# Kernel tuning notes

Hardware: AMD Instinct MI355X
Metric: run time of the kernel (lower is better)

The kernel has to match this reference:

```python
import jax, jax.numpy as jnp
import numpy as np

C = 32            # multiplicity per irrep (node irreps = 32x0e + 32x1o)
N_NODES = 50000
N_EDGES = 800000
R_DIM = 8         # radial embedding dim
R_HID = 8         # radial MLP hidden width
N_SPECIES = 5
AVG_NEIGH = 16.0
N_PATHS = 4       # 0ex0e->0e, 0ex1o->1o, 1ox0e->1o, 1ox1o->0e


def setup_inputs() -> dict:
    key = jax.random.key(0)
    ks = jax.random.split(key, 16)
    inp = {
        'node_features': jax.random.normal(ks[0], (N_NODES, 4 * C), jnp.float32),
        'edge_features': jax.random.normal(ks[1], (N_EDGES, 4), jnp.float32),
        'radial_embedding': jax.random.normal(ks[2], (N_EDGES, R_DIM), jnp.float32),
        'senders': jax.random.randint(ks[3], (N_EDGES,), 0, N_NODES),
        'receivers': jax.random.randint(ks[4], (N_EDGES,), 0, N_NODES),
        'node_species': jax.random.randint(ks[5], (N_NODES,), 0, N_SPECIES),
        # linear_up: per-irrep (block-diagonal) mixing
        'W_up_s': jax.random.normal(ks[6], (C, C), jnp.float32),
        'W_up_v': jax.random.normal(ks[7], (C, C), jnp.float32),
        # radial MLP (no biases, e3nn-style): R_DIM -> R_HID -> N_PATHS*C
        'W_r1': jax.random.normal(ks[8], (R_DIM, R_HID), jnp.float32),
        'W_r2': jax.random.normal(ks[9], (R_HID, N_PATHS * C), jnp.float32),
        # linear_down: 2C x 0e -> 2C (C feats + C gates); 2C x 1o -> C x 1o
        'W_down_s': jax.random.normal(ks[10], (2 * C, 2 * C), jnp.float32),
        'W_down_v': jax.random.normal(ks[11], (2 * C, C), jnp.float32),
        # species-indexed skip connection to gate irreps
        'W_skip_s': jax.random.normal(ks[12], (N_SPECIES, C, 2 * C), jnp.float32),
        'W_skip_v': jax.random.normal(ks[13], (N_SPECIES, C, C), jnp.float32),
    }
    return inp


def reference(node_features, edge_features, radial_embedding, senders, receivers,
              node_species, W_up_s, W_up_v, W_r1, W_r2, W_down_s, W_down_v,
              W_skip_s, W_skip_v):
    N = node_features.shape[0]
    inv_sqrt_C = 1.0 / np.sqrt(C)
    # split irreps: scalars [N,C] and vectors [N,C,3]
    s = node_features[:, :C]
    v = node_features[:, C:].reshape(N, C, 3)
    # ---- linear_up (block-diagonal irreps Linear, fan-in normalized) ----
    s_up = (s @ W_up_s) * inv_sqrt_C
    v_up = jnp.einsum('ncx,cd->ndx', v, W_up_v) * inv_sqrt_C
    # ---- radial MLP -> per-edge tensor-product path weights ----
    h = jax.nn.silu((radial_embedding @ W_r1) * (1.0 / np.sqrt(R_DIM)))
    w = ((h @ W_r2) * (1.0 / np.sqrt(R_HID))).reshape(-1, N_PATHS, C)  # [E,4,C]
    # ---- tensor product messages over edges ----
    sh0 = edge_features[:, 0]      # [E]  l=0
    sh1 = edge_features[:, 1:4]    # [E,3] l=1
    se = s_up[senders]             # [E,C]
    ve = v_up[senders]             # [E,C,3]
    m0 = jnp.concatenate([
        w[:, 0] * se * sh0[:, None],                                      # 0e x 0e -> 0e
        w[:, 3] * jnp.einsum('ecx,ex->ec', ve, sh1) * (1.0 / np.sqrt(3.0))  # 1o x 1o -> 0e
    ], axis=1)                                                            # [E,2C]
    m1 = jnp.concatenate([
        w[:, 1, :, None] * se[:, :, None] * sh1[:, None, :],              # 0e x 1o -> 1o
        w[:, 2, :, None] * ve * sh0[:, None, None],                       # 1o x 0e -> 1o
    ], axis=1)                                                            # [E,2C,3]
    # ---- scatter aggregate to receivers, normalize by sqrt(avg neigh) ----
    inv_sqrt_deg = 1.0 / np.sqrt(AVG_NEIGH)
    agg0 = jax.ops.segment_sum(m0, receivers, num_segments=N) * inv_sqrt_deg
    agg1 = jax.ops.segment_sum(m1, receivers, num_segments=N) * inv_sqrt_deg
    # ---- linear_down to gate irreps (2C x 0e: C feats + C gates; C x 1o) ----
    inv_sqrt_2C = 1.0 / np.sqrt(2 * C)
    sc = (agg0 @ W_down_s) * inv_sqrt_2C                     # [N,2C]
    vc = jnp.einsum('ncx,cd->ndx', agg1, W_down_v) * inv_sqrt_2C  # [N,C,3]
    # ---- species-indexed skip connection ----
    skip_s = jnp.einsum('nc,ncd->nd', s, W_skip_s[node_species]) * inv_sqrt_C
    skip_v = jnp.einsum('ncx,ncd->ndx', v, W_skip_v[node_species]) * inv_sqrt_C
    sc = 0.5 * (sc + skip_s)
    vc = 0.5 * (vc + skip_v)
    # ---- gated nonlinearity: silu on scalars, silu(gates) * vectors ----
    feats = jax.nn.silu(sc[:, :C])
    gates = jax.nn.silu(sc[:, C:])
    vg = vc * gates[:, :, None]
    return jnp.concatenate([feats, vg.reshape(N, 3 * C)], axis=1)  # [N,4C]
```

## Files before the change

kernel.cpp:

```cpp
#include <hip/hip_runtime.h>
#include <stdint.h>

__device__ __forceinline__ float b2f(unsigned short u) {
    union { uint32_t i; float f; } v; v.i = ((uint32_t)u) << 16; return v.f;
}
__device__ __forceinline__ unsigned short f2b(float f) {
    union { float f; uint32_t i; } v; v.f = f;
    uint32_t i = v.i;
    uint32_t r = (i + 0x7fffu + ((i >> 16) & 1u)) >> 16;
    return (unsigned short)r;
}
__device__ __forceinline__ float silu_f(float x) { return x / (1.f + __expf(-x)); }

template<bool BF>
__device__ __forceinline__ float ldin(const void* p, size_t i) {
    if (BF) return b2f(((const unsigned short*)p)[i]);
    return ((const float*)p)[i];
}
template<bool BF>
__device__ __forceinline__ void ld4(const void* p, size_t i, float o[4]) {
    if (BF) {
        const ushort4 u = *(const ushort4*)((const unsigned short*)p + i);
        o[0] = b2f(u.x); o[1] = b2f(u.y); o[2] = b2f(u.z); o[3] = b2f(u.w);
    } else {
        const float4 f = *(const float4*)((const float*)p + i);
        o[0] = f.x; o[1] = f.y; o[2] = f.z; o[3] = f.w;
    }
}
template<bool BF>
__device__ __forceinline__ void stout(void* p, size_t i, float v) {
    if (BF) ((unsigned short*)p)[i] = f2b(v);
    else    ((float*)p)[i] = v;
}

#define INV_SQRT_C   0.17677669529663687f
#define INV_SQRT_8   0.3535533905932738f
#define INV_SQRT_3   0.5773502691896258f
#define INV_SQRT_DEG 0.25f
#define INV_SQRT_2C  0.125f

__device__ __forceinline__ bool detect_bf(const void* nf) {
    const int lane = threadIdx.x & 63;
    const uint32_t w = ((const uint32_t*)nf)[lane];
    const uint32_t ex = (w >> 7) & 0xFFu;
    const unsigned long long m = __ballot(ex >= 96u && ex <= 130u);
    return __popcll(m) > 32;
}

template<bool BF>
__device__ __forceinline__ void prep_body(
    const void* __restrict__ nf, const void* __restrict__ Wus,
    const void* __restrict__ Wuv, const void* __restrict__ radial,
    const int* __restrict__ recv, const void* __restrict__ Wr1,
    unsigned short* __restrict__ stage, unsigned short* __restrict__ hbuf,
    int* __restrict__ counts, int* __restrict__ table,
    int* __restrict__ ovcnt, int* __restrict__ ovlist, int N, int E)
{
    __shared__ float wsm[4][128];
    const int wave = threadIdx.x >> 6;
    const int lane = threadIdx.x & 63;
    const int nwaves = gridDim.x * 4;
    for (int n = blockIdx.x * 4 + wave; n < N; n += nwaves) {
        wsm[wave][lane]      = ldin<BF>(nf, (size_t)n * 128 + lane);
        wsm[wave][64 + lane] = ldin<BF>(nf, (size_t)n * 128 + 64 + lane);
        if (lane < 32) {
            float acc = 0.f;
            #pragma unroll 8
            for (int c = 0; c < 32; ++c) acc += wsm[wave][c] * ldin<BF>(Wus, c * 32 + lane);
            stage[(size_t)n * 160 + lane] = f2b(acc * INV_SQRT_C);
        } else {
            const int dd = lane - 32;
            float ax = 0.f, ay = 0.f, az = 0.f;
            #pragma unroll 8
            for (int c = 0; c < 32; ++c) {
                const float wv = ldin<BF>(Wuv, c * 32 + dd);
                ax += wsm[wave][32 + 3 * c    ] * wv;
                ay += wsm[wave][32 + 3 * c + 1] * wv;
                az += wsm[wave][32 + 3 * c + 2] * wv;
            }
            *(ushort4*)(stage + (size_t)n * 160 + 32 + 4 * dd) =
                make_ushort4(f2b(ax * INV_SQRT_C), f2b(ay * INV_SQRT_C),
                             f2b(az * INV_SQRT_C), (unsigned short)0);
        }
    }
    for (int e = blockIdx.x * 256 + threadIdx.x; e < E; e += gridDim.x * 256) {
        const int rr = recv[e];
        const int pos = atomicAdd(&counts[rr], 1);
        float r[8];
        ld4<BF>(radial, (size_t)e * 8, r);
        ld4<BF>(radial, (size_t)e * 8 + 4, r + 4);
        unsigned short h[8];
        #pragma unroll
        for (int j = 0; j < 8; ++j) {
            float pre = 0.f;
            #pragma unroll
            for (int k = 0; k < 8; ++k) pre += r[k] * ldin<BF>(Wr1, k * 8 + j);
            h[j] = f2b(silu_f(pre * INV_SQRT_8) * INV_SQRT_8);
        }
        ushort4* hp = (ushort4*)(hbuf + (size_t)e * 8);
        hp[0] = make_ushort4(h[0], h[1], h[2], h[3]);
        hp[1] = make_ushort4(h[4], h[5], h[6], h[7]);
        if (pos < 64) table[(size_t)rr * 64 + pos] = e;
        else          ovlist[atomicAdd(ovcnt, 1)] = e;
    }
}
__global__ __launch_bounds__(256) void k_prep(
    const void* nf, const void* Wus, const void* Wuv, const void* radial,
    const int* recv, const void* Wr1,
    unsigned short* stage, unsigned short* hbuf,
    int* counts, int* table, int* ovcnt, int* ovlist, int N, int E)
{
    if (detect_bf(nf)) prep_body<true >(nf, Wus, Wuv, radial, recv, Wr1, stage, hbuf,
                                        counts, table, ovcnt, ovlist, N, E);
    else               prep_body<false>(nf, Wus, Wuv, radial, recv, Wr1, stage, hbuf,
                                        counts, table, ovcnt, ovlist, N, E);
}

template<bool BF>
__device__ __forceinline__ void aggregate_body(
    const void* __restrict__ nf, const void* __restrict__ ef,
    const int* __restrict__ senders, const int* __restrict__ recv,
    const int* __restrict__ species,
    const void* __restrict__ Wr2, const void* __restrict__ Wds,
    const void* __restrict__ Wdv, const void* __restrict__ Wss,
    const void* __restrict__ Wsv,
    const unsigned short* __restrict__ stage,
    const unsigned short* __restrict__ hbuf,
    const int* __restrict__ counts, const int* __restrict__ table,
    const int* __restrict__ ovcnt, const int* __restrict__ ovlist,
    void* __restrict__ out, int N)
{
    __shared__ float ldsM[4][64][16];
    __shared__ float ldsNF[4][128];
    const int wave = threadIdx.x >> 6;
    const int lane = threadIdx.x & 63;
    const int n = blockIdx.x * 4 + wave;
    const bool valid = (n < N);
    const int d = lane - 32;
    int sp = 0, cnt = 0, mc = 0;
    float wA[8], wB[8];
    float acc0 = 0.f, a1x = 0.f, a1y = 0.f, a1z = 0.f;

    if (valid) {
        sp  = species[n];
        cnt = counts[n];
        mc  = (cnt < 64) ? cnt : 64;
        const int colA = (lane < 32) ? lane : lane + 32;
        #pragma unroll
        for (int j = 0; j < 8; ++j) {
            wA[j] = ldin<BF>(Wr2, j * 128 + colA);
            wB[j] = ldin<BF>(Wr2, j * 128 + colA + 32);
        }
        ldsNF[wave][lane]      = ldin<BF>(nf, (size_t)n * 128 + lane);
        ldsNF[wave][64 + lane] = ldin<BF>(nf, (size_t)n * 128 + 64 + lane);
        if (lane < mc) {
            const int eid = table[(size_t)n * 64 + lane];
            const int snd = senders[eid];
            float e4[4];
            if (BF) {
                const ushort4 u = *(const ushort4*)((const unsigned short*)ef + (size_t)eid * 4);
                e4[0] = b2f(u.x); e4[1] = b2f(u.y); e4[2] = b2f(u.z); e4[3] = b2f(u.w);
            } else {
                ld4<false>(ef, (size_t)eid * 4, e4);
            }
            const uint4 th = *(const uint4*)(hbuf + (size_t)eid * 8);
            float* M = ldsM[wave][lane];
            ((float4*)M)[0] = make_float4(e4[0], e4[1], e4[2], e4[3]);
            ((float4*)M)[1] = make_float4(b2f((unsigned short)(th.x & 0xFFFFu)),
                                          b2f((unsigned short)(th.x >> 16)),
                                          b2f((unsigned short)(th.y & 0xFFFFu)),
                                          b2f((unsigned short)(th.y >> 16)));
            ((float4*)M)[2] = make_float4(b2f((unsigned short)(th.z & 0xFFFFu)),
                                          b2f((unsigned short)(th.z >> 16)),
                                          b2f((unsigned short)(th.w & 0xFFFFu)),
                                          b2f((unsigned short)(th.w >> 16)));
            M[12] = __int_as_float(snd);
        }
    }

    if (valid && mc > 0) {
        auto gather = [&](int idx) -> ushort4 {
            const int snd = __float_as_int(ldsM[wave][idx][12]);
            const unsigned short* rec = stage + (size_t)snd * 160;
            if (lane < 32) return make_ushort4(rec[lane], (unsigned short)0,
                                               (unsigned short)0, (unsigned short)0);
            return *(const ushort4*)(rec + 32 + 4 * d);
        };
        ushort4 c0 = make_ushort4(0, 0, 0, 0), c1 = c0, c2 = c0;
        c0 = gather(0);
        if (mc > 1) c1 = gather(1);
        for (int i = 0; i < mc; ++i) {
            if (i + 2 < mc) c2 = gather(i + 2);
            const float4 e4 = ((const float4*)ldsM[wave][i])[0];
            const float4 ha = ((const float4*)ldsM[wave][i])[1];
            const float4 hb = ((const float4*)ldsM[wave][i])[2];
            const float vA = ha.x * wA[0] + ha.y * wA[1] + ha.z * wA[2] + ha.w * wA[3]
                           + hb.x * wA[4] + hb.y * wA[5] + hb.z * wA[6] + hb.w * wA[7];
            const float vB = ha.x * wB[0] + ha.y * wB[1] + ha.z * wB[2] + ha.w * wB[3]
                           + hb.x * wB[4] + hb.y * wB[5] + hb.z * wB[6] + hb.w * wB[7];
            const float sh0 = e4.x, s1x = e4.y, s1y = e4.z, s1z = e4.w;
            if (lane < 32) {
                const float se = b2f(c0.x);
                acc0 += vA * se * sh0;
                const float tt = vB * se;
                a1x += tt * s1x; a1y += tt * s1y; a1z += tt * s1z;
            } else {
                const float vx = b2f(c0.x), vy = b2f(c0.y), vz = b2f(c0.z);
                acc0 += vB * (vx * s1x + vy * s1y + vz * s1z) * INV_SQRT_3;
                const float tt = vA * sh0;
                a1x += tt * vx; a1y += tt * vy; a1z += tt * vz;
            }
            c0 = c1; c1 = c2;
        }
    }
    if (valid && cnt > 64) {
        const int oc = *ovcnt;
        for (int i2 = 0; i2 < oc; ++i2) {
            const int e = ovlist[i2];
            if (recv[e] != n) continue;
            const int s = senders[e];
            float efv[4];
            ld4<BF>(ef, (size_t)e * 4, efv);
            const float sh0 = efv[0], s1x = efv[1], s1y = efv[2], s1z = efv[3];
            float h[8];
            #pragma unroll
            for (int j = 0; j < 8; ++j) h[j] = b2f(hbuf[(size_t)e * 8 + j]);
            const float vA = h[0] * wA[0] + h[1] * wA[1] + h[2] * wA[2] + h[3] * wA[3]
                           + h[4] * wA[4] + h[5] * wA[5] + h[6] * wA[6] + h[7] * wA[7];
            const float vB = h[0] * wB[0] + h[1] * wB[1] + h[2] * wB[2] + h[3] * wB[3]
                           + h[4] * wB[4] + h[5] * wB[5] + h[6] * wB[6] + h[7] * wB[7];
            const unsigned short* rec = stage + (size_t)s * 160;
            if (lane < 32) {
                const float se = b2f(rec[lane]);
                acc0 += vA * se * sh0;
                const float tt = vB * se;
                a1x += tt * s1x; a1y += tt * s1y; a1z += tt * s1z;
            } else {
                const ushort4 u = *(const ushort4*)(rec + 32 + 4 * d);
                const float vx = b2f(u.x), vy = b2f(u.y), vz = b2f(u.z);
                acc0 += vB * (vx * s1x + vy * s1y + vz * s1z) * INV_SQRT_3;
                const float tt = vA * sh0;
                a1x += tt * vx; a1y += tt * vy; a1z += tt * vz;
            }
        }
    }

    __syncthreads();

    float* base = &ldsM[0][0][0];
    float (*lds_agg0)[64]    = (float(*)[64])   base;
    float (*lds_agg1)[3][65] = (float(*)[3][65])(base + 256);
    float (*lds_scf)[64]     = (float(*)[64])  (base + 1036);

    if (valid) {
        lds_agg0[wave][lane]    = acc0 * INV_SQRT_DEG;
        lds_agg1[wave][0][lane] = a1x * INV_SQRT_DEG;
        lds_agg1[wave][1][lane] = a1y * INV_SQRT_DEG;
        lds_agg1[wave][2][lane] = a1z * INV_SQRT_DEG;

        float sc = 0.f;
        #pragma unroll 8
        for (int c = 0; c < 64; ++c) sc += lds_agg0[wave][c] * ldin<BF>(Wds, c * 64 + lane);
        sc *= INV_SQRT_2C;
        float ss = 0.f;
        #pragma unroll 8
        for (int c = 0; c < 32; ++c)
            ss += ldsNF[wave][c] * ldin<BF>(Wss, (size_t)sp * 2048 + c * 64 + lane);
        ss *= INV_SQRT_C;
        lds_scf[wave][lane] = 0.5f * (sc + ss);

        #pragma unroll
        for (int rr = 0; rr < 2; ++rr) {
            const int p = lane + rr * 64;
            float outv;
            if (p < 32) {
                outv = silu_f(lds_scf[wave][p]);
            } else {
                const int o = p - 32;
                const int c = o / 3;
                const int x = o - 3 * c;
                float vc = 0.f;
                #pragma unroll 8
                for (int c2 = 0; c2 < 64; ++c2)
                    vc += lds_agg1[wave][x][c2] * ldin<BF>(Wdv, c2 * 32 + c);
                vc *= INV_SQRT_2C;
                float sv = 0.f;
                #pragma unroll 8
                for (int c2 = 0; c2 < 32; ++c2)
                    sv += ldsNF[wave][32 + c2 * 3 + x] * ldin<BF>(Wsv, (size_t)sp * 1024 + c2 * 32 + c);
                sv *= INV_SQRT_C;
                const float g = silu_f(lds_scf[wave][32 + c]);
                outv = 0.5f * (vc + sv) * g;
            }
            stout<BF>(out, (size_t)n * 128 + p, outv);
        }
    }
}
__global__ __launch_bounds__(256) void k_aggregate(
    const void* nf, const void* ef, const int* senders, const int* recv,
    const int* species,
    const void* Wr2, const void* Wds, const void* Wdv, const void* Wss, const void* Wsv,
    const unsigned short* stage, const unsigned short* hbuf,
    const int* counts, const int* table, const int* ovcnt, const int* ovlist,
    void* out, int N)
{
    if (detect_bf(nf)) aggregate_body<true >(nf, ef, senders, recv, species,
                                             Wr2, Wds, Wdv, Wss, Wsv,
                                             stage, hbuf, counts, table, ovcnt, ovlist, out, N);
    else               aggregate_body<false>(nf, ef, senders, recv, species,
                                             Wr2, Wds, Wdv, Wss, Wsv,
                                             stage, hbuf, counts, table, ovcnt, ovlist, out, N);
}

extern "C" void kernel_launch(void* const* d_in, const int* in_sizes, int n_in,
                              void* d_out, int out_size, void* d_ws, size_t ws_size,
                              hipStream_t stream) {
    const void* nf      = d_in[0];
    const void* ef      = d_in[1];
    const void* radial  = d_in[2];
    const int*  senders = (const int*)d_in[3];
    const int*  recv    = (const int*)d_in[4];
    const int*  specie  = (const int*)d_in[5];
    const void* Wus = d_in[6];
    const void* Wuv = d_in[7];
    const void* Wr1 = d_in[8];
    const void* Wr2 = d_in[9];
    const void* Wds = d_in[10];
    const void* Wdv = d_in[11];
    const void* Wss = d_in[12];
    const void* Wsv = d_in[13];

    const int N = in_sizes[5];
    const int E = in_sizes[3];

    const size_t stageB = (size_t)N * 160 * 2;
    const size_t hbufB  = (size_t)E * 8 * 2;
    const size_t tableB = (size_t)N * 64 * 4;
    const size_t need   = stageB + hbufB + tableB + (size_t)(N + 1 + E) * 4;
    if (ws_size < need) return;

    char* ws = (char*)d_ws;
    unsigned short* stage = (unsigned short*)ws;
    unsigned short* hbuf  = (unsigned short*)(ws + stageB);
    int* table   = (int*)(ws + stageB + hbufB);
    int* counts  = (int*)(ws + stageB + hbufB + tableB);
    int* ovcnt   = counts + N;
    int* ovlist  = ovcnt + 1;

    hipMemsetAsync(counts, 0, (size_t)(N + 1) * sizeof(int), stream);

    k_prep<<<2048, 256, 0, stream>>>(nf, Wus, Wuv, radial, recv, Wr1,
                                     stage, hbuf, counts, table, ovcnt, ovlist, N, E);
    k_aggregate<<<(N + 3) / 4, 256, 0, stream>>>(nf, ef, senders, recv, specie,
                                                 Wr2, Wds, Wdv, Wss, Wsv,
                                                 stage, hbuf, counts, table, ovcnt, ovlist,
                                                 d_out, N);
}
```

Before: 479.9 us.

## Split prep into node/edge kernels, shrink staging layout, batch sender gathers

```diff
diff --git a/kernel.cpp b/kernel.cpp
--- a/kernel.cpp
+++ b/kernel.cpp
@@ -39,81 +39,99 @@
 #define INV_SQRT_DEG 0.25f
 #define INV_SQRT_2C  0.125f
 
-__device__ __forceinline__ bool detect_bf(const void* nf) {
+__device__ __forceinline__ bool detect_bf(const void* buf) {
     const int lane = threadIdx.x & 63;
-    const uint32_t w = ((const uint32_t*)nf)[lane];
+    const uint32_t w = ((const uint32_t*)buf)[lane];
     const uint32_t ex = (w >> 7) & 0xFFu;
     const unsigned long long m = __ballot(ex >= 96u && ex <= 130u);
     return __popcll(m) > 32;
 }
 
 template<bool BF>
-__device__ __forceinline__ void prep_body(
+__device__ __forceinline__ void prep_nodes_body(
     const void* __restrict__ nf, const void* __restrict__ Wus,
-    const void* __restrict__ Wuv, const void* __restrict__ radial,
-    const int* __restrict__ recv, const void* __restrict__ Wr1,
-    unsigned short* __restrict__ stage, unsigned short* __restrict__ hbuf,
-    int* __restrict__ counts, int* __restrict__ table,
-    int* __restrict__ ovcnt, int* __restrict__ ovlist, int N, int E)
-{
-    __shared__ float wsm[4][128];
+    const void* __restrict__ Wuv, unsigned short* __restrict__ stage,
+    int N, float* smem)
+{
+    float (*wsm)[128] = (float(*)[128])smem;
     const int wave = threadIdx.x >> 6;
     const int lane = threadIdx.x & 63;
-    const int nwaves = gridDim.x * 4;
-    for (int n = blockIdx.x * 4 + wave; n < N; n += nwaves) {
-        wsm[wave][lane]      = ldin<BF>(nf, (size_t)n * 128 + lane);
-        wsm[wave][64 + lane] = ldin<BF>(nf, (size_t)n * 128 + 64 + lane);
-        if (lane < 32) {
-            float acc = 0.f;
-            #pragma unroll 8
-            for (int c = 0; c < 32; ++c) acc += wsm[wave][c] * ldin<BF>(Wus, c * 32 + lane);
-            stage[(size_t)n * 160 + lane] = f2b(acc * INV_SQRT_C);
-        } else {
-            const int dd = lane - 32;
-            float ax = 0.f, ay = 0.f, az = 0.f;
-            #pragma unroll 8
-            for (int c = 0; c < 32; ++c) {
-                const float wv = ldin<BF>(Wuv, c * 32 + dd);
-                ax += wsm[wave][32 + 3 * c    ] * wv;
-                ay += wsm[wave][32 + 3 * c + 1] * wv;
-                az += wsm[wave][32 + 3 * c + 2] * wv;
-            }
-            *(ushort4*)(stage + (size_t)n * 160 + 32 + 4 * dd) =
-                make_ushort4(f2b(ax * INV_SQRT_C), f2b(ay * INV_SQRT_C),
-                             f2b(az * INV_SQRT_C), (unsigned short)0);
-        }
-    }
-    for (int e = blockIdx.x * 256 + threadIdx.x; e < E; e += gridDim.x * 256) {
-        const int rr = recv[e];
-        const int pos = atomicAdd(&counts[rr], 1);
-        float r[8];
-        ld4<BF>(radial, (size_t)e * 8, r);
-        ld4<BF>(radial, (size_t)e * 8 + 4, r + 4);
-        unsigned short h[8];
+    const int n = blockIdx.x * 4 + wave;
+    if (n >= N) return;
+    wsm[wave][lane]      = ldin<BF>(nf, (size_t)n * 128 + lane);
+    wsm[wave][64 + lane] = ldin<BF>(nf, (size_t)n * 128 + 64 + lane);
+    if (lane < 32) {
+        float acc = 0.f;
+        #pragma unroll 8
+        for (int c = 0; c < 32; ++c) acc += wsm[wave][c] * ldin<BF>(Wus, c * 32 + lane);
+        stage[(size_t)n * 128 + lane] = f2b(acc * INV_SQRT_C);
+    } else {
+        const int dd = lane - 32;
+        float ax = 0.f, ay = 0.f, az = 0.f;
+        #pragma unroll 8
+        for (int c = 0; c < 32; ++c) {
+            const float wv = ldin<BF>(Wuv, c * 32 + dd);
+            ax += wsm[wave][32 + 3 * c    ] * wv;
+            ay += wsm[wave][32 + 3 * c + 1] * wv;
+            az += wsm[wave][32 + 3 * c + 2] * wv;
+        }
+        stage[(size_t)n * 128 + 32 + dd] = f2b(ax * INV_SQRT_C);
+        stage[(size_t)n * 128 + 64 + dd] = f2b(ay * INV_SQRT_C);
+        stage[(size_t)n * 128 + 96 + dd] = f2b(az * INV_SQRT_C);
+    }
+}
+__global__ __launch_bounds__(256) void k_prep_nodes(
+    const void* nf, const void* Wus, const void* Wuv,
+    unsigned short* stage, int N)
+{
+    __shared__ float smem[4 * 128];
+    if (detect_bf(nf)) prep_nodes_body<true >(nf, Wus, Wuv, stage, N, smem);
+    else               prep_nodes_body<false>(nf, Wus, Wuv, stage, N, smem);
+}
+
+template<bool BF>
+__device__ __forceinline__ void prep_edges_body(
+    const void* __restrict__ radial, const int* __restrict__ senders,
+    const int* __restrict__ recv, const void* __restrict__ Wr1,
+    unsigned short* __restrict__ hbuf, int* __restrict__ counts,
+    int* __restrict__ table, int* __restrict__ tableS,
+    int* __restrict__ ovcnt, int* __restrict__ ovlist, int E)
+{
+    const int e = blockIdx.x * 256 + threadIdx.x;
+    if (e >= E) return;
+    const int rr  = recv[e];
+    const int snd = senders[e];
+    const int pos = atomicAdd(&counts[rr], 1);
+    float r[8];
+    ld4<BF>(radial, (size_t)e * 8, r);
+    ld4<BF>(radial, (size_t)e * 8 + 4, r + 4);
+    unsigned short h[8];
+    #pragma unroll
+    for (int j = 0; j < 8; ++j) {
+        float pre = 0.f;
         #pragma unroll
-        for (int j = 0; j < 8; ++j) {
-            float pre = 0.f;
-            #pragma unroll
-            for (int k = 0; k < 8; ++k) pre += r[k] * ldin<BF>(Wr1, k * 8 + j);
-            h[j] = f2b(silu_f(pre * INV_SQRT_8) * INV_SQRT_8);
-        }
-        ushort4* hp = (ushort4*)(hbuf + (size_t)e * 8);
-        hp[0] = make_ushort4(h[0], h[1], h[2], h[3]);
-        hp[1] = make_ushort4(h[4], h[5], h[6], h[7]);
-        if (pos < 64) table[(size_t)rr * 64 + pos] = e;
-        else          ovlist[atomicAdd(ovcnt, 1)] = e;
-    }
-}
-__global__ __launch_bounds__(256) void k_prep(
-    const void* nf, const void* Wus, const void* Wuv, const void* radial,
-    const int* recv, const void* Wr1,
-    unsigned short* stage, unsigned short* hbuf,
-    int* counts, int* table, int* ovcnt, int* ovlist, int N, int E)
-{
-    if (detect_bf(nf)) prep_body<true >(nf, Wus, Wuv, radial, recv, Wr1, stage, hbuf,
-                                        counts, table, ovcnt, ovlist, N, E);
-    else               prep_body<false>(nf, Wus, Wuv, radial, recv, Wr1, stage, hbuf,
-                                        counts, table, ovcnt, ovlist, N, E);
+        for (int k = 0; k < 8; ++k) pre += r[k] * ldin<BF>(Wr1, k * 8 + j);
+        h[j] = f2b(silu_f(pre * INV_SQRT_8) * INV_SQRT_8);
+    }
+    ushort4* hp = (ushort4*)(hbuf + (size_t)e * 8);
+    hp[0] = make_ushort4(h[0], h[1], h[2], h[3]);
+    hp[1] = make_ushort4(h[4], h[5], h[6], h[7]);
+    if (pos < 64) {
+        table[(size_t)rr * 64 + pos] = e;
+        if (tableS) tableS[(size_t)rr * 64 + pos] = snd;
+    } else {
+        ovlist[atomicAdd(ovcnt, 1)] = e;
+    }
+}
+__global__ __launch_bounds__(256) void k_prep_edges(
+    const void* radial, const int* senders, const int* recv, const void* Wr1,
+    unsigned short* hbuf, int* counts, int* table, int* tableS,
+    int* ovcnt, int* ovlist, int E)
+{
+    if (detect_bf(radial)) prep_edges_body<true >(radial, senders, recv, Wr1, hbuf,
+                                                  counts, table, tableS, ovcnt, ovlist, E);
+    else                   prep_edges_body<false>(radial, senders, recv, Wr1, hbuf,
+                                                  counts, table, tableS, ovcnt, ovlist, E);
 }
 
 template<bool BF>
@@ -127,11 +145,12 @@
     const unsigned short* __restrict__ stage,
     const unsigned short* __restrict__ hbuf,
     const int* __restrict__ counts, const int* __restrict__ table,
+    const int* __restrict__ tableS,
     const int* __restrict__ ovcnt, const int* __restrict__ ovlist,
-    void* __restrict__ out, int N)
-{
-    __shared__ float ldsM[4][64][16];
-    __shared__ float ldsNF[4][128];
+    void* __restrict__ out, int N, float* smem)
+{
+    float (*ldsM)[64][16] = (float(*)[64][16])smem;
+    float (*ldsNF)[128]   = (float(*)[128])(smem + 4096);
     const int wave = threadIdx.x >> 6;
     const int lane = threadIdx.x & 63;
     const int n = blockIdx.x * 4 + wave;
@@ -155,7 +174,8 @@
         ldsNF[wave][64 + lane] = ldin<BF>(nf, (size_t)n * 128 + 64 + lane);
         if (lane < mc) {
             const int eid = table[(size_t)n * 64 + lane];
-            const int snd = senders[eid];
+            const int snd = tableS ? tableS[(size_t)n * 64 + lane]
+                                   : senders[eid];
             float e4[4];
             if (BF) {
                 const ushort4 u = *(const ushort4*)((const unsigned short*)ef + (size_t)eid * 4);
@@ -179,38 +199,48 @@
     }
 
     if (valid && mc > 0) {
-        auto gather = [&](int idx) -> ushort4 {
+        auto gatherOne = [&](int idx, unsigned short& o0, unsigned short& o1,
+                             unsigned short& o2) {
             const int snd = __float_as_int(ldsM[wave][idx][12]);
-            const unsigned short* rec = stage + (size_t)snd * 160;
-            if (lane < 32) return make_ushort4(rec[lane], (unsigned short)0,
-                                               (unsigned short)0, (unsigned short)0);
-            return *(const ushort4*)(rec + 32 + 4 * d);
+            const unsigned short* rec = stage + (size_t)snd * 128;
+            if (lane < 32) { o0 = rec[lane]; }
+            else { o0 = rec[32 + d]; o1 = rec[64 + d]; o2 = rec[96 + d]; }
         };
-        ushort4 c0 = make_ushort4(0, 0, 0, 0), c1 = c0, c2 = c0;
-        c0 = gather(0);
-        if (mc > 1) c1 = gather(1);
-        for (int i = 0; i < mc; ++i) {
-            if (i + 2 < mc) c2 = gather(i + 2);
-            const float4 e4 = ((const float4*)ldsM[wave][i])[0];
-            const float4 ha = ((const float4*)ldsM[wave][i])[1];
-            const float4 hb = ((const float4*)ldsM[wave][i])[2];
+        auto edgeC = [&](int i, unsigned short s0, unsigned short s1,
+                         unsigned short s2) {
+            const float4 e4 = *((const float4*)&ldsM[wave][i][0]);
+            const float4 ha = *((const float4*)&ldsM[wave][i][4]);
+            const float4 hb = *((const float4*)&ldsM[wave][i][8]);
             const float vA = ha.x * wA[0] + ha.y * wA[1] + ha.z * wA[2] + ha.w * wA[3]
                            + hb.x * wA[4] + hb.y * wA[5] + hb.z * wA[6] + hb.w * wA[7];
             const float vB = ha.x * wB[0] + ha.y * wB[1] + ha.z * wB[2] + ha.w * wB[3]
                            + hb.x * wB[4] + hb.y * wB[5] + hb.z * wB[6] + hb.w * wB[7];
-            const float sh0 = e4.x, s1x = e4.y, s1y = e4.z, s1z = e4.w;
             if (lane < 32) {
-                const float se = b2f(c0.x);
-                acc0 += vA * se * sh0;
+                const float se = b2f(s0);
+                acc0 += vA * se * e4.x;
                 const float tt = vB * se;
-                a1x += tt * s1x; a1y += tt * s1y; a1z += tt * s1z;
+                a1x += tt * e4.y; a1y += tt * e4.z; a1z += tt * e4.w;
             } else {
-                const float vx = b2f(c0.x), vy = b2f(c0.y), vz = b2f(c0.z);
-                acc0 += vB * (vx * s1x + vy * s1y + vz * s1z) * INV_SQRT_3;
-                const float tt = vA * sh0;
+                const float vx = b2f(s0), vy = b2f(s1), vz = b2f(s2);
+                acc0 += vB * (vx * e4.y + vy * e4.z + vz * e4.w);
+                const float tt = vA * e4.x;
                 a1x += tt * vx; a1y += tt * vy; a1z += tt * vz;
             }
-            c0 = c1; c1 = c2;
+        };
+        unsigned short g0[8], g1[8], g2[8];
+        int base = 0;
+        for (; base + 8 <= mc; base += 8) {
+            #pragma unroll
+            for (int k = 0; k < 8; ++k) gatherOne(base + k, g0[k], g1[k], g2[k]);
+            #pragma unroll
+            for (int k = 0; k < 8; ++k) edgeC(base + k, g0[k], g1[k], g2[k]);
+        }
+        if (base < mc) {
+            const int bc = mc - base;
+            #pragma unroll
+            for (int k = 0; k < 7; ++k) if (k < bc) gatherOne(base + k, g0[k], g1[k], g2[k]);
+            #pragma unroll
+            for (int k = 0; k < 7; ++k) if (k < bc) edgeC(base + k, g0[k], g1[k], g2[k]);
         }
     }
     if (valid && cnt > 64) {
@@ -229,28 +259,28 @@
                            + h[4] * wA[4] + h[5] * wA[5] + h[6] * wA[6] + h[7] * wA[7];
             const float vB = h[0] * wB[0] + h[1] * wB[1] + h[2] * wB[2] + h[3] * wB[3]
                            + h[4] * wB[4] + h[5] * wB[5] + h[6] * wB[6] + h[7] * wB[7];
-            const unsigned short* rec = stage + (size_t)s * 160;
+            const unsigned short* rec = stage + (size_t)s * 128;
             if (lane < 32) {
                 const float se = b2f(rec[lane]);
                 acc0 += vA * se * sh0;
                 const float tt = vB * se;
                 a1x += tt * s1x; a1y += tt * s1y; a1z += tt * s1z;
             } else {
-                const ushort4 u = *(const ushort4*)(rec + 32 + 4 * d);
-                const float vx = b2f(u.x), vy = b2f(u.y), vz = b2f(u.z);
-                acc0 += vB * (vx * s1x + vy * s1y + vz * s1z) * INV_SQRT_3;
+                const float vx = b2f(rec[32 + d]), vy = b2f(rec[64 + d]), vz = b2f(rec[96 + d]);
+                acc0 += vB * (vx * s1x + vy * s1y + vz * s1z);
                 const float tt = vA * sh0;
                 a1x += tt * vx; a1y += tt * vy; a1z += tt * vz;
             }
         }
     }
+    if (valid && lane >= 32) acc0 *= INV_SQRT_3;
 
     __syncthreads();
 
-    float* base = &ldsM[0][0][0];
-    float (*lds_agg0)[64]    = (float(*)[64])   base;
-    float (*lds_agg1)[3][65] = (float(*)[3][65])(base + 256);
-    float (*lds_scf)[64]     = (float(*)[64])  (base + 1036);
+    float* base_ = smem;
+    float (*lds_agg0)[64]    = (float(*)[64])   base_;
+    float (*lds_agg1)[3][65] = (float(*)[3][65])(base_ + 256);
+    float (*lds_scf)[64]     = (float(*)[64])  (base_ + 1036);
 
     if (valid) {
         lds_agg0[wave][lane]    = acc0 * INV_SQRT_DEG;
@@ -301,15 +331,19 @@
     const int* species,
     const void* Wr2, const void* Wds, const void* Wdv, const void* Wss, const void* Wsv,
     const unsigned short* stage, const unsigned short* hbuf,
-    const int* counts, const int* table, const int* ovcnt, const int* ovlist,
+    const int* counts, const int* table, const int* tableS,
+    const int* ovcnt, const int* ovlist,
     void* out, int N)
 {
+    __shared__ float smem[4 * 64 * 16 + 4 * 128];
     if (detect_bf(nf)) aggregate_body<true >(nf, ef, senders, recv, species,
                                              Wr2, Wds, Wdv, Wss, Wsv,
-                                             stage, hbuf, counts, table, ovcnt, ovlist, out, N);
+                                             stage, hbuf, counts, table, tableS,
+                                             ovcnt, ovlist, out, N, smem);
     else               aggregate_body<false>(nf, ef, senders, recv, species,
                                              Wr2, Wds, Wdv, Wss, Wsv,
-                                             stage, hbuf, counts, table, ovcnt, ovlist, out, N);
+                                             stage, hbuf, counts, table, tableS,
+                                             ovcnt, ovlist, out, N, smem);
 }
 
 extern "C" void kernel_launch(void* const* d_in, const int* in_sizes, int n_in,
@@ -333,26 +367,33 @@
     const int N = in_sizes[5];
     const int E = in_sizes[3];
 
-    const size_t stageB = (size_t)N * 160 * 2;
+    const size_t stageB = (size_t)N * 128 * 2;
     const size_t hbufB  = (size_t)E * 8 * 2;
     const size_t tableB = (size_t)N * 64 * 4;
-    const size_t need   = stageB + hbufB + tableB + (size_t)(N + 1 + E) * 4;
-    if (ws_size < need) return;
+    const size_t miscB  = (size_t)(N + 1 + E) * 4;
+    const size_t need1  = stageB + hbufB + tableB + miscB;
+    const size_t need2  = need1 + tableB;
+    if (ws_size < need1) return;
 
     char* ws = (char*)d_ws;
     unsigned short* stage = (unsigned short*)ws;
     unsigned short* hbuf  = (unsigned short*)(ws + stageB);
-    int* table   = (int*)(ws + stageB + hbufB);
-    int* counts  = (int*)(ws + stageB + hbufB + tableB);
-    int* ovcnt   = counts + N;
-    int* ovlist  = ovcnt + 1;
+    int* table = (int*)(ws + stageB + hbufB);
+    size_t off = stageB + hbufB + tableB;
+    int* tableS = nullptr;
+    if (ws_size >= need2) { tableS = (int*)(ws + off); off += tableB; }
+    int* counts = (int*)(ws + off);
+    int* ovcnt  = counts + N;
+    int* ovlist = ovcnt + 1;
 
     hipMemsetAsync(counts, 0, (size_t)(N + 1) * sizeof(int), stream);
 
-    k_prep<<<2048, 256, 0, stream>>>(nf, Wus, Wuv, radial, recv, Wr1,
-                                     stage, hbuf, counts, table, ovcnt, ovlist, N, E);
+    k_prep_nodes<<<(N + 3) / 4, 256, 0, stream>>>(nf, Wus, Wuv, stage, N);
+    k_prep_edges<<<(E + 255) / 256, 256, 0, stream>>>(radial, senders, recv, Wr1,
+                                                      hbuf, counts, table, tableS,
+                                                      ovcnt, ovlist, E);
     k_aggregate<<<(N + 3) / 4, 256, 0, stream>>>(nf, ef, senders, recv, specie,
                                                  Wr2, Wds, Wdv, Wss, Wsv,
-                                                 stage, hbuf, counts, table, ovcnt, ovlist,
-                                                 d_out, N);
-}
+                                                 stage, hbuf, counts, table, tableS,
+                                                 ovcnt, ovlist, d_out, N);
+}
```

Measured after the change: 470.2 us. -2.0%, faster.
